# Kernel tuning notes

Measured on AMD Instinct MI355X. Metric: run time of the kernel, lower is better.

Reference implementation:

```python
import jax, jax.numpy as jnp
import numpy as np

N_NODES = 100000


def _mean_agg(x, src, dst, n_nodes):
    # gather source features along edges, segment-sum into destinations, divide by in-degree
    msg = x[src]                                               # [E, D]
    s = jax.ops.segment_sum(msg, dst, num_segments=n_nodes)    # [N, D]
    deg = jax.ops.segment_sum(jnp.ones((src.shape[0],), x.dtype), dst, num_segments=n_nodes)
    return s / jnp.maximum(deg, 1.0)[:, None]


def _sage_layer(x, src, dst, W_self, W_neigh, b, n_nodes):
    h_neigh = _mean_agg(x, src, dst, n_nodes)
    return x @ W_self + h_neigh @ W_neigh + b


def setup_inputs() -> dict:
    key = jax.random.key(0)
    ks = jax.random.split(key, 8)
    in_f, h_f, n_cls = 128, 128, 40
    n_edges = 1600000
    sc = lambda d: 1.0 / np.sqrt(d)
    return {
        "features": jax.random.normal(ks[0], (N_NODES, in_f), dtype=jnp.float32),
        "src": jax.random.randint(ks[1], (n_edges,), 0, N_NODES),
        "dst": jax.random.randint(ks[2], (n_edges,), 0, N_NODES),
        "W1_self": jax.random.normal(ks[3], (in_f, h_f), dtype=jnp.float32) * sc(in_f),
        "W1_neigh": jax.random.normal(ks[4], (in_f, h_f), dtype=jnp.float32) * sc(in_f),
        "b1": jnp.zeros((h_f,), dtype=jnp.float32),
        "W2_self": jax.random.normal(ks[5], (h_f, n_cls), dtype=jnp.float32) * sc(h_f),
        "W2_neigh": jax.random.normal(ks[6], (h_f, n_cls), dtype=jnp.float32) * sc(h_f),
        "b2": jnp.zeros((n_cls,), dtype=jnp.float32),
    }


def reference(features, src, dst, W1_self, W1_neigh, b1, W2_self, W2_neigh, b2):
    h = _sage_layer(features, src, dst, W1_self, W1_neigh, b1, N_NODES)
    h = jax.nn.relu(h)
    h = _sage_layer(h, src, dst, W2_self, W2_neigh, b2, N_NODES)
    return h
```

## Files before the change

kernel.cpp:

```cpp
#include <hip/hip_runtime.h>


typedef __attribute__((ext_vector_type(8))) short bf16x8;
typedef __attribute__((ext_vector_type(4))) float f32x4;
typedef __attribute__((ext_vector_type(2))) float f32x2;

#define BIN_SHIFT 7
#define BIN_SIZE  128
#define NB        256

#define OFF_ROWSTART (1ull << 20)
#define OFF_HIST     (2ull << 20)
#define OFF_SCAN     (3ull << 20)
#define OFF_BSUMS    (4ull << 20)
#define OFF_BOFFS    ((4ull << 20) + (64ull << 10))
#define OFF_PACKED   (5ull << 20)
#define OFF_CSR      (12ull << 20)
#define OFF_W1T      (19ull << 20)
#define OFF_W2T      (20ull << 20)
#define OFF_XB       (21ull << 20)
#define OFF_XQ       (47ull << 20)
#define OFF_AGGB     (61ull << 20)
#define OFF_T2       (87ull << 20)

static __device__ __forceinline__ unsigned short f2b(float f) {
    unsigned int u = __float_as_uint(f);
    u += 0x7fffu + ((u >> 16) & 1u);
    return (unsigned short)(u >> 16);
}
static __device__ __forceinline__ float blo(unsigned int v) { return __uint_as_float(v << 16); }
static __device__ __forceinline__ float bhi(unsigned int v) { return __uint_as_float(v & 0xffff0000u); }


__global__ __launch_bounds__(256) void cast_hist(
    const float* __restrict__ x,
    const float* __restrict__ W1s, const float* __restrict__ W1n,
    const float* __restrict__ W2s, const float* __restrict__ W2n,
    unsigned short* __restrict__ xb, unsigned char* __restrict__ xq,
    unsigned short* __restrict__ W1t, unsigned short* __restrict__ W2t,
    unsigned short* __restrict__ t2,
    const int* __restrict__ dst, int* __restrict__ hist,
    int n16, int castBlocks, int castPlus, int N, int E, int nbins) {
    __shared__ int h[1024];
    int blk = blockIdx.x, t = threadIdx.x;
    if (blk >= castPlus) {
        int b = blk - castPlus;
        for (int i = t; i < nbins; i += 256) h[i] = 0;
        __syncthreads();
        int chunk = (E + NB - 1) / NB;
        int base = b * chunk;
        int lim = min(base + chunk, E);
        for (int e = base + t; e < lim; e += 256)
            atomicAdd(&h[dst[e] >> BIN_SHIFT], 1);
        __syncthreads();
        for (int i = t; i < nbins; i += 256)
            hist[i * NB + b] = h[i];
        return;
    }
    if (blk < castBlocks) {
        int i = blk * 256 + t;
        if (i >= n16) return;
        const float4* p = (const float4*)x + (size_t)i * 4;
        float4 v0 = p[0], v1 = p[1], v2 = p[2], v3 = p[3];
        float f[16] = {v0.x, v0.y, v0.z, v0.w, v1.x, v1.y, v1.z, v1.w,
                       v2.x, v2.y, v2.z, v2.w, v3.x, v3.y, v3.z, v3.w};
        unsigned short ob[16];
#pragma unroll
        for (int k = 0; k < 16; k++) ob[k] = f2b(f[k]);
        *(float4*)(xb + (size_t)i * 16) = *(float4*)&ob[0];
        *(float4*)(xb + (size_t)i * 16 + 8) = *(float4*)&ob[8];
        unsigned int w[4];
#pragma unroll
        for (int k = 0; k < 4; k++) {
            int u = __builtin_amdgcn_cvt_pk_fp8_f32(f[4 * k + 0], f[4 * k + 1], 0, false);
            u = __builtin_amdgcn_cvt_pk_fp8_f32(f[4 * k + 2], f[4 * k + 3], u, true);
            w[k] = (unsigned int)u;
        }
        *(uint4*)(xq + (size_t)i * 16) = *(uint4*)w;
    } else if (blk < castBlocks + 128) {
        int c = blk - castBlocks;
        float v = (t < 128) ? W1s[(size_t)t * 128 + c] : W1n[(size_t)(t - 128) * 128 + c];
        W1t[(size_t)c * 256 + t] = f2b(v);
    } else if (blk < castBlocks + 208) {
        if (t < 128) {
            int c = blk - castBlocks - 128;
            float v = (c < 40) ? W2s[(size_t)t * 40 + c] : W2n[(size_t)t * 40 + (c - 40)];
            W2t[(size_t)c * 128 + t] = f2b(v);
        }
    } else {
        if (t < 32) ((unsigned int*)(xq + (size_t)N * 128))[t] = 0u;
        else if (t < 64) ((unsigned int*)(t2 + (size_t)N * 64))[t - 32] = 0u;
    }
}


__global__ void scan1(const int* __restrict__ in, int* __restrict__ tmp,
                      int* __restrict__ bsums, int M) {
    __shared__ int s[256];
    int t = threadIdx.x;
    int i = blockIdx.x * 256 + t;
    int v = (i < M) ? in[i] : 0;
    s[t] = v;
    __syncthreads();
    for (int off = 1; off < 256; off <<= 1) {
        int u = (t >= off) ? s[t - off] : 0;
        __syncthreads();
        s[t] += u;
        __syncthreads();
    }
    if (i < M) tmp[i] = s[t] - v;
    if (t == 255) bsums[blockIdx.x] = s[t];
}

__global__ void scan2(const int* __restrict__ bsums, int* __restrict__ boffs, int nb) {
    __shared__ int s[1024];
    int t = threadIdx.x;
    int v = (t < nb) ? bsums[t] : 0;
    s[t] = v;
    __syncthreads();
    for (int off = 1; off < 1024; off <<= 1) {
        int u = (t >= off) ? s[t - off] : 0;
        __syncthreads();
        s[t] += u;
        __syncthreads();
    }
    if (t < nb) boffs[t] = s[t] - v;
}

__global__ __launch_bounds__(256) void scatter_det(
    const int* __restrict__ src, const int* __restrict__ dst,
    const int* __restrict__ tmp, const int* __restrict__ boffs,
    unsigned int* __restrict__ packed, int E, int nbins) {
    __shared__ int cur[1024];
    int b = blockIdx.x, t = threadIdx.x;
    for (int i = t; i < nbins; i += 256) cur[i] = tmp[i * NB + b] + boffs[i];
    __syncthreads();
    int chunk = (E + NB - 1) / NB;
    int base = b * chunk;
    int lim = min(base + chunk, E);
    for (int e = base + t; e < lim; e += 256) {
        int d = dst[e];
        int bin = d >> BIN_SHIFT;
        int pos = atomicAdd(&cur[bin], 1);
        packed[pos] = ((unsigned int)(d & (BIN_SIZE - 1)) << 20) | (unsigned int)src[e];
    }
}

__global__ __launch_bounds__(256) void bin_fill(
    const unsigned int* __restrict__ packed, const int* __restrict__ tmp,
    const int* __restrict__ boffs,
    int* __restrict__ row_start, int* __restrict__ csr_src, int N, int nbins, int E) {
    __shared__ int cnt[BIN_SIZE];
    __shared__ int pre[BIN_SIZE];
    __shared__ int ex[BIN_SIZE];
    int b = blockIdx.x;
    int t = threadIdx.x;
    int node0 = b << BIN_SHIFT;
    int beg = tmp[b * NB] + boffs[b];
    int end = (b + 1 < nbins) ? (tmp[(b + 1) * NB] + boffs[b + 1]) : E;

    if (t < BIN_SIZE) cnt[t] = 0;
    __syncthreads();
    for (int i = beg + t; i < end; i += 256)
        atomicAdd(&cnt[packed[i] >> 20], 1);
    __syncthreads();
    if (t < BIN_SIZE) pre[t] = cnt[t];
    __syncthreads();
    for (int off = 1; off < BIN_SIZE; off <<= 1) {
        int u = (t < BIN_SIZE && t >= off) ? pre[t - off] : 0;
        __syncthreads();
        if (t < BIN_SIZE) pre[t] += u;
        __syncthreads();
    }
    if (t < BIN_SIZE) {
        ex[t] = pre[t] - cnt[t];
        int node = node0 + t;
        if (node < N) row_start[node] = beg + ex[t];
        cnt[t] = 0;
    }
    if (b == nbins - 1 && t == 0) row_start[N] = E;
    __syncthreads();
    for (int i = beg + t; i < end; i += 256) {
        unsigned int p = packed[i];
        int dl = p >> 20;
        int s = p & 0xFFFFF;
        int ofs = atomicAdd(&cnt[dl], 1);
        csr_src[beg + ex[dl] + ofs] = s;
    }
}


__global__ void agg_mean_fp8(const unsigned char* __restrict__ xq,
                             const int* __restrict__ row_start,
                             const int* __restrict__ csr_src,
                             unsigned short* __restrict__ aggb, int N) {
    int wv = (blockIdx.x * blockDim.x + threadIdx.x) >> 6;
    int lane = threadIdx.x & 63;
    if (2 * wv >= N) return;
    int node = 2 * wv + (lane >> 5);
    bool valid = node < N;
    int hl = lane & 31;
    int g = hl >> 4;
    int l = hl & 15;
    int beg = valid ? row_start[node] : 0;
    int end = valid ? row_start[node + 1] : 0;
    const char* xbase = (const char*)xq;
    unsigned loff = (unsigned)l << 3;

    float a[8];
#pragma unroll
    for (int k = 0; k < 8; k++) a[k] = 0.f;

    for (int e = beg; e < end; e += 16) {
        int s[8];
#pragma unroll
        for (int k = 0; k < 8; k++) {
            int ee = e + 2 * k + g;
            int idx = csr_src[min(ee, end - 1)];
            s[k] = (ee < end) ? idx : N;
        }
#pragma unroll
        for (int k = 0; k < 8; k++) {
            uint2 v = *(const uint2*)(xbase + (((unsigned)s[k] << 7) + loff));
            f32x2 p0 = __builtin_amdgcn_cvt_pk_f32_fp8(v.x, false);
            f32x2 p1 = __builtin_amdgcn_cvt_pk_f32_fp8(v.x, true);
            f32x2 p2 = __builtin_amdgcn_cvt_pk_f32_fp8(v.y, false);
            f32x2 p3 = __builtin_amdgcn_cvt_pk_f32_fp8(v.y, true);
            a[0] += p0.x; a[1] += p0.y; a[2] += p1.x; a[3] += p1.y;
            a[4] += p2.x; a[5] += p2.y; a[6] += p3.x; a[7] += p3.y;
        }
    }

#pragma unroll
    for (int k = 0; k < 8; k++)
        a[k] += __shfl_xor(a[k], 16);
    if (g == 0 && valid) {
        float inv = 1.0f / fmaxf((float)(end - beg), 1.0f);
        unsigned int ow[4];
#pragma unroll
        for (int k = 0; k < 4; k++)
            ow[k] = (unsigned int)f2b(a[2 * k] * inv) |
                    ((unsigned int)f2b(a[2 * k + 1] * inv) << 16);
        *(uint4*)((char*)aggb + (((unsigned)node << 8) + ((unsigned)l << 4))) = *(uint4*)ow;
    }
}

__global__ void agg2_add(const unsigned short* __restrict__ t2,
                         const int* __restrict__ row_start,
                         const int* __restrict__ csr_src, const float* __restrict__ b2,
                         float* __restrict__ out, int N) {
    int wv = (blockIdx.x * blockDim.x + threadIdx.x) >> 6;
    int lane = threadIdx.x & 63;
    if (2 * wv >= N) return;
    int node = 2 * wv + (lane >> 5);
    bool valid = node < N;
    int hl = lane & 31;
    int g = hl >> 4;
    int l = hl & 15;
    int beg = valid ? row_start[node] : 0;
    int end = valid ? row_start[node + 1] : 0;
    const char* tb = (const char*)t2;
    bool active = (l < 10);
    unsigned loff = (unsigned)l << 3;

    float a0 = 0.f, a1 = 0.f, a2 = 0.f, a3 = 0.f;

    for (int e = beg; e < end; e += 16) {
        int s[8];
#pragma unroll
        for (int k = 0; k < 8; k++) {
            int ee = e + 2 * k + g;
            int idx = csr_src[min(ee, end - 1)];
            s[k] = (ee < end) ? idx : N;
        }
        if (active) {
#pragma unroll
            for (int k = 0; k < 8; k++) {
                uint2 v = *(const uint2*)(tb + (((unsigned)s[k] << 7) + loff));
                a0 += blo(v.x); a1 += bhi(v.x);
                a2 += blo(v.y); a3 += bhi(v.y);
            }
        }
    }

    a0 += __shfl_xor(a0, 16);
    a1 += __shfl_xor(a1, 16);
    a2 += __shfl_xor(a2, 16);
    a3 += __shfl_xor(a3, 16);
    if (g == 0 && active && valid) {
        float inv = 1.0f / fmaxf((float)(end - beg), 1.0f);
        float4 bb = ((const float4*)b2)[l];
        float4* op = (float4*)((char*)out + ((unsigned)node * 160u + ((unsigned)l << 4)));
        float4 cur = *op;
        cur.x += a0 * inv + bb.x;
        cur.y += a1 * inv + bb.y;
        cur.z += a2 * inv + bb.z;
        cur.w += a3 * inv + bb.w;
        *op = cur;
    }
}


__global__ __launch_bounds__(256) void gemm12_mfma(
    const unsigned short* __restrict__ xb, const unsigned short* __restrict__ aggb,
    const unsigned short* __restrict__ W1t, const unsigned short* __restrict__ W2t,
    const float* __restrict__ b1, float* __restrict__ out,
    unsigned short* __restrict__ t2, int N) {

    __shared__ unsigned short As[128 * 40];
    __shared__ unsigned short Bs[128 * 40];
    __shared__ unsigned short Hs[128 * 136];
    __shared__ unsigned short B2[80 * 136];

    int tid = threadIdx.x;
    int wave = tid >> 6, lane = tid & 63;
    int row0 = blockIdx.x * 128;
    int m = lane & 15, quad = lane >> 4;

    for (int idx = tid; idx < 1280; idx += 256) {
        int r = idx >> 4, seg = idx & 15;
        *(float4*)&B2[r * 136 + seg * 8] = *(const float4*)(W2t + (size_t)r * 128 + seg * 8);
    }

    f32x4 acc[2][8];
#pragma unroll
    for (int i = 0; i < 2; i++)
#pragma unroll
        for (int j = 0; j < 8; j++) acc[i][j] = (f32x4){0.f, 0.f, 0.f, 0.f};

    for (int k0 = 0; k0 < 256; k0 += 32) {
        __syncthreads();
        {
            int r = tid >> 1, kk = (tid & 1) * 16;
            int row = row0 + r;
            float4 v0 = make_float4(0, 0, 0, 0), v1 = v0;
            if (row < N) {
                const unsigned short* s = (k0 < 128)
                    ? (xb + (size_t)row * 128 + k0 + kk)
                    : (aggb + (size_t)row * 128 + (k0 - 128) + kk);
                const float4* p = (const float4*)s;
                v0 = p[0]; v1 = p[1];
            }
            *(float4*)&As[r * 40 + kk] = v0;
            *(float4*)&As[r * 40 + kk + 8] = v1;
            const float4* q2 = (const float4*)(W1t + (size_t)r * 256 + k0 + kk);
            float4 w0 = q2[0], w1 = q2[1];
            *(float4*)&Bs[r * 40 + kk] = w0;
            *(float4*)&Bs[r * 40 + kk + 8] = w1;
        }
        __syncthreads();

        bf16x8 af0 = *(bf16x8*)&As[(wave * 32 + m) * 40 + quad * 8];
        bf16x8 af1 = *(bf16x8*)&As[(wave * 32 + 16 + m) * 40 + quad * 8];
#pragma unroll
        for (int j = 0; j < 8; j++) {
            bf16x8 bfg = *(bf16x8*)&Bs[(j * 16 + m) * 40 + quad * 8];
            acc[0][j] = __builtin_amdgcn_mfma_f32_16x16x32_bf16(af0, bfg, acc[0][j], 0, 0, 0);
            acc[1][j] = __builtin_amdgcn_mfma_f32_16x16x32_bf16(af1, bfg, acc[1][j], 0, 0, 0);
        }
    }

#pragma unroll
    for (int j = 0; j < 8; j++) {
        int col = j * 16 + m;
        float bias = b1[col];
#pragma unroll
        for (int i = 0; i < 2; i++) {
#pragma unroll
            for (int r = 0; r < 4; r++) {
                int rl = wave * 32 + i * 16 + quad * 4 + r;
                Hs[rl * 136 + col] = f2b(fmaxf(acc[i][j][r] + bias, 0.f));
            }
        }
    }
    __syncthreads();

    f32x4 acc2[2][5];
#pragma unroll
    for (int i = 0; i < 2; i++)
#pragma unroll
        for (int j = 0; j < 5; j++) acc2[i][j] = (f32x4){0.f, 0.f, 0.f, 0.f};

#pragma unroll
    for (int k0 = 0; k0 < 128; k0 += 32) {
        bf16x8 af0 = *(bf16x8*)&Hs[(wave * 32 + m) * 136 + k0 + quad * 8];
        bf16x8 af1 = *(bf16x8*)&Hs[(wave * 32 + 16 + m) * 136 + k0 + quad * 8];
#pragma unroll
        for (int j = 0; j < 5; j++) {
            bf16x8 bfg = *(bf16x8*)&B2[(j * 16 + m) * 136 + k0 + quad * 8];
            acc2[0][j] = __builtin_amdgcn_mfma_f32_16x16x32_bf16(af0, bfg, acc2[0][j], 0, 0, 0);
            acc2[1][j] = __builtin_amdgcn_mfma_f32_16x16x32_bf16(af1, bfg, acc2[1][j], 0, 0, 0);
        }
    }

#pragma unroll
    for (int j = 0; j < 5; j++) {
        int col = j * 16 + m;
#pragma unroll
        for (int i = 0; i < 2; i++) {
#pragma unroll
            for (int r = 0; r < 4; r++) {
                int row = row0 + wave * 32 + i * 16 + quad * 4 + r;
                if (row < N) {
                    float v = acc2[i][j][r];
                    if (col < 40) {
                        out[(size_t)row * 40 + col] = v;
                    } else {
                        t2[(size_t)row * 64 + (col - 40)] = f2b(v);
                    }
                }
            }
        }
    }
}


extern "C" void kernel_launch(void* const* d_in, const int* in_sizes, int n_in,
                              void* d_out, int out_size, void* d_ws, size_t ws_size,
                              hipStream_t stream) {
    const float* x   = (const float*)d_in[0];
    const int*   src = (const int*)d_in[1];
    const int*   dst = (const int*)d_in[2];
    const float* W1s = (const float*)d_in[3];
    const float* W1n = (const float*)d_in[4];
    const float* b1  = (const float*)d_in[5];
    const float* W2s = (const float*)d_in[6];
    const float* W2n = (const float*)d_in[7];
    const float* b2  = (const float*)d_in[8];
    float* out = (float*)d_out;

    int N = in_sizes[0] / 128;
    int E = in_sizes[1];
    int nbins = (N + BIN_SIZE - 1) / BIN_SIZE;
    int M = nbins * NB;

    char* ws = (char*)d_ws;
    int*            row_start  = (int*)(ws + OFF_ROWSTART);
    int*            hist       = (int*)(ws + OFF_HIST);
    int*            scanned    = (int*)(ws + OFF_SCAN);
    int*            bsums      = (int*)(ws + OFF_BSUMS);
    int*            boffs      = (int*)(ws + OFF_BOFFS);
    unsigned int*   packed     = (unsigned int*)(ws + OFF_PACKED);
    int*            csr_src    = (int*)(ws + OFF_CSR);
    unsigned short* W1t        = (unsigned short*)(ws + OFF_W1T);
    unsigned short* W2t        = (unsigned short*)(ws + OFF_W2T);
    unsigned short* xb         = (unsigned short*)(ws + OFF_XB);
    unsigned char*  xq         = (unsigned char*)(ws + OFF_XQ);
    unsigned short* aggb       = (unsigned short*)(ws + OFF_AGGB);
    unsigned short* t2         = (unsigned short*)(ws + OFF_T2);

    int scanBlocks = (M + 255) / 256;

    int n16 = N * 128 / 16;
    int castBlocks = (n16 + 255) / 256;
    int castPlus = castBlocks + 128 + 80 + 1;

    cast_hist<<<castPlus + NB, 256, 0, stream>>>(
        x, W1s, W1n, W2s, W2n, xb, xq, W1t, W2t, t2,
        dst, hist, n16, castBlocks, castPlus, N, E, nbins);
    scan1<<<scanBlocks, 256, 0, stream>>>(hist, scanned, bsums, M);
    scan2<<<1, 1024, 0, stream>>>(bsums, boffs, scanBlocks);
    scatter_det<<<NB, 256, 0, stream>>>(src, dst, scanned, boffs, packed, E, nbins);
    bin_fill<<<nbins, 256, 0, stream>>>(packed, scanned, boffs, row_start, csr_src, N, nbins, E);

    int nodePairs = (N + 1) / 2;
    int aggBlocks = (nodePairs * 64 + 255) / 256;
    agg_mean_fp8<<<aggBlocks, 256, 0, stream>>>(xq, row_start, csr_src, aggb, N);
    gemm12_mfma<<<(N + 127) / 128, 256, 0, stream>>>(xb, aggb, W1t, W2t, b1, out, t2, N);
    agg2_add<<<aggBlocks, 256, 0, stream>>>(t2, row_start, csr_src, b2, out, N);
}
```

Before: 275.3 us.

## Build CSR with per-node global atomic degree count and direct scatter

Measured after the change: 414.1 us. 50.4% more time.

```diff
diff --git a/kernel.cpp b/kernel.cpp
--- a/kernel.cpp
+++ b/kernel.cpp
@@ -5,16 +5,14 @@
 typedef __attribute__((ext_vector_type(4))) float f32x4;
 typedef __attribute__((ext_vector_type(2))) float f32x2;
 
-#define BIN_SHIFT 7
-#define BIN_SIZE  128
-#define NB        256
+#define NB 256
 
 #define OFF_ROWSTART (1ull << 20)
-#define OFF_HIST     (2ull << 20)
+#define OFF_DEG      (2ull << 20)
 #define OFF_SCAN     (3ull << 20)
 #define OFF_BSUMS    (4ull << 20)
 #define OFF_BOFFS    ((4ull << 20) + (64ull << 10))
-#define OFF_PACKED   (5ull << 20)
+#define OFF_CURSOR   (5ull << 20)
 #define OFF_CSR      (12ull << 20)
 #define OFF_W1T      (19ull << 20)
 #define OFF_W2T      (20ull << 20)
@@ -32,29 +30,23 @@
 static __device__ __forceinline__ float bhi(unsigned int v) { return __uint_as_float(v & 0xffff0000u); }
 
 
-__global__ __launch_bounds__(256) void cast_hist(
+__global__ __launch_bounds__(256) void cast_deg(
     const float* __restrict__ x,
     const float* __restrict__ W1s, const float* __restrict__ W1n,
     const float* __restrict__ W2s, const float* __restrict__ W2n,
     unsigned short* __restrict__ xb, unsigned char* __restrict__ xq,
     unsigned short* __restrict__ W1t, unsigned short* __restrict__ W2t,
     unsigned short* __restrict__ t2,
-    const int* __restrict__ dst, int* __restrict__ hist,
-    int n16, int castBlocks, int castPlus, int N, int E, int nbins) {
-    __shared__ int h[1024];
+    const int* __restrict__ dst, int* __restrict__ deg,
+    int n16, int castBlocks, int castPlus, int N, int E) {
     int blk = blockIdx.x, t = threadIdx.x;
     if (blk >= castPlus) {
         int b = blk - castPlus;
-        for (int i = t; i < nbins; i += 256) h[i] = 0;
-        __syncthreads();
         int chunk = (E + NB - 1) / NB;
         int base = b * chunk;
         int lim = min(base + chunk, E);
         for (int e = base + t; e < lim; e += 256)
-            atomicAdd(&h[dst[e] >> BIN_SHIFT], 1);
-        __syncthreads();
-        for (int i = t; i < nbins; i += 256)
-            hist[i * NB + b] = h[i];
+            atomicAdd(&deg[dst[e]], 1);
         return;
     }
     if (blk < castBlocks) {
@@ -127,65 +119,26 @@
     if (t < nb) boffs[t] = s[t] - v;
 }
 
-__global__ __launch_bounds__(256) void scatter_det(
+__global__ void finish_rs(const int* __restrict__ tmp, const int* __restrict__ boffs,
+                          int* __restrict__ row_start, int* __restrict__ cursor,
+                          int N, int E) {
+    int i = blockIdx.x * 256 + threadIdx.x;
+    if (i < N) {
+        int v = tmp[i] + boffs[i >> 8];
+        row_start[i] = v;
+        cursor[i] = v;
+    }
+    if (i == N) row_start[N] = E;
+}
+
+__global__ __launch_bounds__(256) void scatter_direct(
     const int* __restrict__ src, const int* __restrict__ dst,
-    const int* __restrict__ tmp, const int* __restrict__ boffs,
-    unsigned int* __restrict__ packed, int E, int nbins) {
-    __shared__ int cur[1024];
-    int b = blockIdx.x, t = threadIdx.x;
-    for (int i = t; i < nbins; i += 256) cur[i] = tmp[i * NB + b] + boffs[i];
-    __syncthreads();
-    int chunk = (E + NB - 1) / NB;
-    int base = b * chunk;
-    int lim = min(base + chunk, E);
-    for (int e = base + t; e < lim; e += 256) {
+    int* __restrict__ cursor, int* __restrict__ csr_src, int E) {
+    int stride = gridDim.x * 256;
+    for (int e = blockIdx.x * 256 + threadIdx.x; e < E; e += stride) {
         int d = dst[e];
-        int bin = d >> BIN_SHIFT;
-        int pos = atomicAdd(&cur[bin], 1);
-        packed[pos] = ((unsigned int)(d & (BIN_SIZE - 1)) << 20) | (unsigned int)src[e];
-    }
-}
-
-__global__ __launch_bounds__(256) void bin_fill(
-    const unsigned int* __restrict__ packed, const int* __restrict__ tmp,
-    const int* __restrict__ boffs,
-    int* __restrict__ row_start, int* __restrict__ csr_src, int N, int nbins, int E) {
-    __shared__ int cnt[BIN_SIZE];
-    __shared__ int pre[BIN_SIZE];
-    __shared__ int ex[BIN_SIZE];
-    int b = blockIdx.x;
-    int t = threadIdx.x;
-    int node0 = b << BIN_SHIFT;
-    int beg = tmp[b * NB] + boffs[b];
-    int end = (b + 1 < nbins) ? (tmp[(b + 1) * NB] + boffs[b + 1]) : E;
-
-    if (t < BIN_SIZE) cnt[t] = 0;
-    __syncthreads();
-    for (int i = beg + t; i < end; i += 256)
-        atomicAdd(&cnt[packed[i] >> 20], 1);
-    __syncthreads();
-    if (t < BIN_SIZE) pre[t] = cnt[t];
-    __syncthreads();
-    for (int off = 1; off < BIN_SIZE; off <<= 1) {
-        int u = (t < BIN_SIZE && t >= off) ? pre[t - off] : 0;
-        __syncthreads();
-        if (t < BIN_SIZE) pre[t] += u;
-        __syncthreads();
-    }
-    if (t < BIN_SIZE) {
-        ex[t] = pre[t] - cnt[t];
-        int node = node0 + t;
-        if (node < N) row_start[node] = beg + ex[t];
-        cnt[t] = 0;
-    }
-    if (b == nbins - 1 && t == 0) row_start[N] = E;
-    __syncthreads();
-    for (int i = beg + t; i < end; i += 256) {
-        unsigned int p = packed[i];
-        int dl = p >> 20;
-        int s = p & 0xFFFFF;
-        int ofs = atomicAdd(&cnt[dl], 1);
-        csr_src[beg + ex[dl] + ofs] = s;
+        int pos = atomicAdd(&cursor[d], 1);
+        csr_src[pos] = src[e];
     }
 }
 
@@ -431,16 +384,14 @@
 
     int N = in_sizes[0] / 128;
     int E = in_sizes[1];
-    int nbins = (N + BIN_SIZE - 1) / BIN_SIZE;
-    int M = nbins * NB;
 
     char* ws = (char*)d_ws;
     int*            row_start  = (int*)(ws + OFF_ROWSTART);
-    int*            hist       = (int*)(ws + OFF_HIST);
+    int*            deg        = (int*)(ws + OFF_DEG);
     int*            scanned    = (int*)(ws + OFF_SCAN);
     int*            bsums      = (int*)(ws + OFF_BSUMS);
     int*            boffs      = (int*)(ws + OFF_BOFFS);
-    unsigned int*   packed     = (unsigned int*)(ws + OFF_PACKED);
+    int*            cursor     = (int*)(ws + OFF_CURSOR);
     int*            csr_src    = (int*)(ws + OFF_CSR);
     unsigned short* W1t        = (unsigned short*)(ws + OFF_W1T);
     unsigned short* W2t        = (unsigned short*)(ws + OFF_W2T);
@@ -449,19 +400,20 @@
     unsigned short* aggb       = (unsigned short*)(ws + OFF_AGGB);
     unsigned short* t2         = (unsigned short*)(ws + OFF_T2);
 
-    int scanBlocks = (M + 255) / 256;
-
     int n16 = N * 128 / 16;
     int castBlocks = (n16 + 255) / 256;
     int castPlus = castBlocks + 128 + 80 + 1;
-
-    cast_hist<<<castPlus + NB, 256, 0, stream>>>(
+    int scanBlocks = (N + 255) / 256;
+
+    hipMemsetAsync(deg, 0, (size_t)(N + 1) * sizeof(int), stream);
+
+    cast_deg<<<castPlus + NB, 256, 0, stream>>>(
         x, W1s, W1n, W2s, W2n, xb, xq, W1t, W2t, t2,
-        dst, hist, n16, castBlocks, castPlus, N, E, nbins);
-    scan1<<<scanBlocks, 256, 0, stream>>>(hist, scanned, bsums, M);
+        dst, deg, n16, castBlocks, castPlus, N, E);
+    scan1<<<scanBlocks, 256, 0, stream>>>(deg, scanned, bsums, N);
     scan2<<<1, 1024, 0, stream>>>(bsums, boffs, scanBlocks);
-    scatter_det<<<NB, 256, 0, stream>>>(src, dst, scanned, boffs, packed, E, nbins);
-    bin_fill<<<nbins, 256, 0, stream>>>(packed, scanned, boffs, row_start, csr_src, N, nbins, E);
+    finish_rs<<<scanBlocks + 1, 256, 0, stream>>>(scanned, boffs, row_start, cursor, N, E);
+    scatter_direct<<<2048, 256, 0, stream>>>(src, dst, cursor, csr_src, E);
 
     int nodePairs = (N + 1) / 2;
     int aggBlocks = (nodePairs * 64 + 255) / 256;
```
